# Kernel optimization log

Measured on AMD Instinct MI355X. Metric: run time of the kernel, lower is better.

Reference implementation:

```python
import jax, jax.numpy as jnp
import numpy as np

N_NODES = 100000
EPS = 1e-5


def gcn_conv(x, src, dst, W, b):
    # PyG GCNConv: h = W x; out_i = sum_{j->i} norm_ij * h_j  (with self-loops)
    h = x @ W  # [N, out]
    deg = jax.ops.segment_sum(jnp.ones_like(src, dtype=h.dtype), dst,
                              num_segments=N_NODES) + 1.0  # +1 self-loop
    dinv = jax.lax.rsqrt(deg)  # [N]
    norm = dinv[src] * dinv[dst]  # [E]
    msgs = h[src] * norm[:, None]  # [E, out]
    agg = jax.ops.segment_sum(msgs, dst, num_segments=N_NODES)
    agg = agg + h * (1.0 / deg)[:, None]  # self-loop term, norm = deg^-1
    return agg + b


def graph_norm(x, w, b, mean_scale):
    # PyG GraphNorm, single graph: normalize over nodes per feature
    mean = jnp.mean(x, axis=0, keepdims=True)
    xc = x - mean_scale * mean
    var = jnp.mean(xc * xc, axis=0, keepdims=True)
    return w * xc * jax.lax.rsqrt(var + EPS) + b


def layer_norm(x, w, b):
    mean = jnp.mean(x, axis=-1, keepdims=True)
    xc = x - mean
    var = jnp.mean(xc * xc, axis=-1, keepdims=True)
    return w * xc * jax.lax.rsqrt(var + EPS) + b


def setup_inputs() -> dict:
    key = jax.random.key(0)
    ks = jax.random.split(key, 8)
    in_dim, hid, emb = 128, 64, 32
    x = jax.random.normal(ks[0], (N_NODES, in_dim), dtype=jnp.float32)
    edge_index = jax.random.randint(ks[1], (2, 1600000), 0, N_NODES, dtype=jnp.int64)
    s = 0.05
    return {
        'x': x,
        'edge_index': edge_index,
        'W1': jax.random.normal(ks[2], (in_dim, hid), jnp.float32) * s,
        'b1': jnp.zeros((hid,), jnp.float32),
        'W2': jax.random.normal(ks[3], (hid, hid), jnp.float32) * s,
        'b2': jnp.zeros((hid,), jnp.float32),
        'gn_w': jnp.ones((hid,), jnp.float32),
        'gn_b': jnp.zeros((hid,), jnp.float32),
        'gn_ms': jnp.ones((hid,), jnp.float32),
        'ln_w': jnp.ones((hid,), jnp.float32),
        'ln_b': jnp.zeros((hid,), jnp.float32),
        'fc_W': jax.random.normal(ks[4], (hid, emb), jnp.float32) * s,
        'fc_b': jnp.zeros((emb,), jnp.float32),
    }


def reference(x, edge_index, W1, b1, W2, b2, gn_w, gn_b, gn_ms, ln_w, ln_b, fc_W, fc_b):
    src, dst = edge_index[0], edge_index[1]
    h = jax.nn.relu(gcn_conv(x, src, dst, W1, b1))
    h = graph_norm(h, gn_w, gn_b, gn_ms)
    h = layer_norm(h, ln_w, ln_b)
    # dropout: identity in eval mode
    h = jax.nn.relu(gcn_conv(h, src, dst, W2, b2))
    h = graph_norm(h, gn_w, gn_b, gn_ms)
    h = layer_norm(h, ln_w, ln_b)
    pooled = jnp.max(h, axis=0)  # [hid]
    embedding = pooled @ fc_W + fc_b  # [emb]; emb != 1 so no sigmoid
    return embedding
```

## Files before the change

kernel.cpp:

```cpp
#include <hip/hip_runtime.h>
#include <hip/hip_bf16.h>

#define EPSV 1e-5f
#define CHUNK 256
#define CAP 6144
#define MAXNB 512

typedef __attribute__((ext_vector_type(8))) short bf16x8;
typedef __attribute__((ext_vector_type(4))) float f32x4;

__device__ __forceinline__ ushort f2bf(float f) {
    union { float f; unsigned u; } c; c.f = f;
    unsigned u = c.u;
    return (ushort)((u + 0x7fffu + ((u >> 16) & 1u)) >> 16);
}
__device__ __forceinline__ float bf2f(ushort h) {
    union { unsigned u; float f; } c; c.u = ((unsigned)h) << 16;
    return c.f;
}
__device__ __forceinline__ float bflo(unsigned u) {
    union { unsigned u; float f; } c; c.u = u << 16;
    return c.f;
}
__device__ __forceinline__ float bfhi(unsigned u) {
    union { unsigned u; float f; } c; c.u = u & 0xFFFF0000u;
    return c.f;
}
__device__ __forceinline__ void acc8(float* a, uint4 u) {
    a[0] += bflo(u.x); a[1] += bfhi(u.x);
    a[2] += bflo(u.y); a[3] += bfhi(u.y);
    a[4] += bflo(u.z); a[5] += bfhi(u.z);
    a[6] += bflo(u.w); a[7] += bfhi(u.w);
}


__global__ void prep_kernel(const float* __restrict__ W1, const float* __restrict__ W2,
                            ushort* __restrict__ wsw1, ushort* __restrict__ wsw2,
                            int* __restrict__ bcur, int NB) {
    int t = blockIdx.x * blockDim.x + threadIdx.x;
    if (t < 128 * 64) {
        int k = t >> 6, n = t & 63;
        wsw1[((k >> 3) * 64 + n) * 8 + (k & 7)] = f2bf(W1[t]);
    }
    if (t < 64 * 64) {
        int k = t >> 6, n = t & 63;
        wsw2[((k >> 3) * 64 + n) * 8 + (k & 7)] = f2bf(W2[t]);
    }
    if (t < NB) bcur[t] = t * CAP;
}


#define EPB 8192

__global__ void __launch_bounds__(256) bucket_scatter(const int* __restrict__ ei,
                                                      int* __restrict__ bcur,
                                                      unsigned* __restrict__ bdata, int E,
                                                      int NB) {
    __shared__ int h[MAXNB];
    __shared__ int cur[MAXNB];
    int t = threadIdx.x;
    int base = blockIdx.x * EPB;
    int end = min(base + EPB, E);
    for (int b = t; b < NB; b += 256) h[b] = 0;
    __syncthreads();
    for (int e = base + t * 4; e < end; e += 1024) {
        int4 d4 = *reinterpret_cast<const int4*>(&ei[E + e]);
        atomicAdd(&h[d4.x >> 8], 1);
        atomicAdd(&h[d4.y >> 8], 1);
        atomicAdd(&h[d4.z >> 8], 1);
        atomicAdd(&h[d4.w >> 8], 1);
    }
    __syncthreads();
    for (int b = t; b < NB; b += 256) {
        int c = h[b];
        cur[b] = c ? atomicAdd(&bcur[b], c) : 0;
    }
    __syncthreads();
    for (int e = base + t * 4; e < end; e += 1024) {
        int4 s4 = *reinterpret_cast<const int4*>(&ei[e]);
        int4 d4 = *reinterpret_cast<const int4*>(&ei[E + e]);
        int p0 = atomicAdd(&cur[d4.x >> 8], 1);
        bdata[p0] = (unsigned)s4.x | ((unsigned)(d4.x & 255) << 20);
        int p1 = atomicAdd(&cur[d4.y >> 8], 1);
        bdata[p1] = (unsigned)s4.y | ((unsigned)(d4.y & 255) << 20);
        int p2 = atomicAdd(&cur[d4.z >> 8], 1);
        bdata[p2] = (unsigned)s4.z | ((unsigned)(d4.z & 255) << 20);
        int p3 = atomicAdd(&cur[d4.w >> 8], 1);
        bdata[p3] = (unsigned)s4.w | ((unsigned)(d4.w & 255) << 20);
    }
}


__global__ void __launch_bounds__(256) bucket_finish(const unsigned* __restrict__ bdata,
                                                     const int* __restrict__ bcur,
                                                     int2* __restrict__ NI,
                                                     float* __restrict__ dinv,
                                                     int* __restrict__ srcs, int N) {
    __shared__ int h[CHUNK];
    __shared__ int cur[CHUNK];
    int t = threadIdx.x;
    int beg = blockIdx.x * CAP;
    int end = bcur[blockIdx.x];
    h[t] = 0;
    __syncthreads();
    for (int e = beg + t; e < end; e += 256) atomicAdd(&h[bdata[e] >> 20], 1);
    __syncthreads();
    int deg = h[t];
    int pc = (deg + 3) & ~3;
    cur[t] = pc;
    __syncthreads();
    for (int off = 1; off < 256; off <<= 1) {
        int x = (t >= off) ? cur[t - off] : 0;
        __syncthreads();
        cur[t] += x;
        __syncthreads();
    }
    int begp = beg + cur[t] - pc;
    int node = blockIdx.x * CHUNK + t;
    if (node < N) {
        NI[node] = make_int2(begp, pc);
        dinv[node] = rsqrtf((float)deg + 1.0f);
    }
    h[t] = begp;
    __syncthreads();
    for (int e = beg + t; e < end; e += 256) {
        unsigned p = bdata[e];
        int pos = atomicAdd(&h[p >> 20], 1);
        srcs[pos] = (int)((p & 0xFFFFFu) << 3);
    }
    __syncthreads();
    int zr = N * 8;
    for (int k = h[t]; k < begp + pc; k++) srcs[k] = zr;
}


__global__ void __launch_bounds__(256) mm1_kernel(const float* __restrict__ X,
                                                  const ushort* __restrict__ wsw,
                                                  const float* __restrict__ dinv,
                                                  ushort* __restrict__ Ht, int N) {
    const int KO = 4;
    int w = threadIdx.x >> 6, lane = threadIdx.x & 63;
    int m = lane & 15, q = lane >> 4;
    int row = blockIdx.x * 64 + w * 16 + m;

    bf16x8 afrag[KO];
#pragma unroll
    for (int kk = 0; kk < KO; kk++) {
        float xv[8];
        if (row < N) {
            const float4* xp = reinterpret_cast<const float4*>(X + (size_t)row * 128 + kk * 32 + q * 8);
            float4 v0 = xp[0], v1 = xp[1];
            xv[0] = v0.x; xv[1] = v0.y; xv[2] = v0.z; xv[3] = v0.w;
            xv[4] = v1.x; xv[5] = v1.y; xv[6] = v1.z; xv[7] = v1.w;
        } else {
#pragma unroll
            for (int j = 0; j < 8; j++) xv[j] = 0.f;
        }
#pragma unroll
        for (int j = 0; j < 8; j++) afrag[kk][j] = (short)f2bf(xv[j]);
    }

    float dv[4];
#pragma unroll
    for (int reg = 0; reg < 4; reg++) {
        int r = blockIdx.x * 64 + w * 16 + q * 4 + reg;
        dv[reg] = (r < N) ? dinv[r] : 0.f;
    }

    const bf16x8* wp = reinterpret_cast<const bf16x8*>(wsw);
#pragma unroll
    for (int ct = 0; ct < 4; ct++) {
        f32x4 acc = {0.f, 0.f, 0.f, 0.f};
#pragma unroll
        for (int kk = 0; kk < KO; kk++) {
            bf16x8 b = wp[(kk * 4 + q) * 64 + ct * 16 + m];
            acc = __builtin_amdgcn_mfma_f32_16x16x32_bf16(afrag[kk], b, acc, 0, 0, 0);
        }
#pragma unroll
        for (int reg = 0; reg < 4; reg++) {
            int r = blockIdx.x * 64 + w * 16 + q * 4 + reg;
            if (r < N) Ht[(size_t)r * 64 + ct * 16 + m] = f2bf(acc[reg] * dv[reg]);
        }
    }
}


__global__ void __launch_bounds__(256) mm2_kernel(
    const ushort* __restrict__ A2, const ushort* __restrict__ wsw,
    const float* __restrict__ sums, const float* __restrict__ gn_w,
    const float* __restrict__ gn_b, const float* __restrict__ gn_ms,
    const float* __restrict__ ln_w, const float* __restrict__ ln_b,
    const float* __restrict__ dinv, ushort* __restrict__ Ht, int N) {
    __shared__ float sg[64], tg[64], lwv[64], lbv[64];
    int t = threadIdx.x;
    if (t < 64) {
        float invN = 1.0f / (float)N;
        float mean = sums[t] * invN;
        float m2 = sums[64 + t] * invN;
        float ms = gn_ms[t];
        float var = m2 - 2.f * ms * mean * mean + ms * ms * mean * mean;
        float s = gn_w[t] * rsqrtf(var + EPSV);
        sg[t] = s;
        tg[t] = gn_b[t] - s * ms * mean;
        lwv[t] = ln_w[t];
        lbv[t] = ln_b[t];
    }
    __syncthreads();

    int w = t >> 6, lane = t & 63;
    int m = lane & 15, q = lane >> 4;
    int row = blockIdx.x * 64 + w * 16 + m;

    float g[16];
#pragma unroll
    for (int kk = 0; kk < 2; kk++) {
        uint4 u = make_uint4(0, 0, 0, 0);
        if (row < N)
            u = *reinterpret_cast<const uint4*>(A2 + (size_t)row * 64 + kk * 32 + q * 8);
        unsigned uu[4] = {u.x, u.y, u.z, u.w};
#pragma unroll
        for (int p = 0; p < 4; p++) {
            int f0 = kk * 32 + q * 8 + 2 * p;
            g[kk * 8 + 2 * p] = sg[f0] * bflo(uu[p]) + tg[f0];
            g[kk * 8 + 2 * p + 1] = sg[f0 + 1] * bfhi(uu[p]) + tg[f0 + 1];
        }
    }
    float s1 = 0.f;
#pragma unroll
    for (int i = 0; i < 16; i++) s1 += g[i];
    s1 += __shfl_xor(s1, 16);
    s1 += __shfl_xor(s1, 32);
    float mu = s1 * (1.f / 64.f);
    float s2 = 0.f;
#pragma unroll
    for (int i = 0; i < 16; i++) {
        float c = g[i] - mu;
        s2 += c * c;
    }
    s2 += __shfl_xor(s2, 16);
    s2 += __shfl_xor(s2, 32);
    float rs = rsqrtf(s2 * (1.f / 64.f) + EPSV);

    bf16x8 afrag[2];
#pragma unroll
    for (int kk = 0; kk < 2; kk++) {
#pragma unroll
        for (int j = 0; j < 8; j++) {
            int f = kk * 32 + q * 8 + j;
            float y = lwv[f] * (g[kk * 8 + j] - mu) * rs + lbv[f];
            afrag[kk][j] = (short)f2bf(y);
        }
    }

    float dv[4];
#pragma unroll
    for (int reg = 0; reg < 4; reg++) {
        int r = blockIdx.x * 64 + w * 16 + q * 4 + reg;
        dv[reg] = (r < N) ? dinv[r] : 0.f;
    }

    const bf16x8* wp = reinterpret_cast<const bf16x8*>(wsw);
#pragma unroll
    for (int ct = 0; ct < 4; ct++) {
        f32x4 acc = {0.f, 0.f, 0.f, 0.f};
#pragma unroll
        for (int kk = 0; kk < 2; kk++) {
            bf16x8 b = wp[(kk * 4 + q) * 64 + ct * 16 + m];
            acc = __builtin_amdgcn_mfma_f32_16x16x32_bf16(afrag[kk], b, acc, 0, 0, 0);
        }
#pragma unroll
        for (int reg = 0; reg < 4; reg++) {
            int r = blockIdx.x * 64 + w * 16 + q * 4 + reg;
            if (r < N) Ht[(size_t)r * 64 + ct * 16 + m] = f2bf(acc[reg] * dv[reg]);
        }
    }
}


__global__ void __launch_bounds__(256) agg_kernel(
    const ushort* __restrict__ Ht, const int2* __restrict__ NI, const int* __restrict__ srcs,
    const float* __restrict__ dinv, const float* __restrict__ bias,
    ushort* __restrict__ out, float* __restrict__ sums, int N) {
    int t = threadIdx.x;
    int lane = t & 63;
    int g = lane >> 3, fq = lane & 7;
    int wid = (blockIdx.x * blockDim.x + t) >> 6;
    int nw = (gridDim.x * blockDim.x) >> 6;
    const uint4* H4 = reinterpret_cast<const uint4*>(Ht);
    uint4* O4 = reinterpret_cast<uint4*>(out);
    const int ZR = N * 8;
    float bb[8];
#pragma unroll
    for (int j = 0; j < 8; j++) bb[j] = bias[fq * 8 + j];
    float ps1[8] = {0, 0, 0, 0, 0, 0, 0, 0}, ps2[8] = {0, 0, 0, 0, 0, 0, 0, 0};

    for (int jo = wid; jo * 8 < N; jo += nw) {
        int node = jo * 8 + g;
        bool valid = node < N;
        int2 info = valid ? NI[node] : make_int2(0, 0);
        float di = valid ? dinv[node] : 0.f;
        int e = info.x, end = info.x + info.y;
        float a[8] = {0, 0, 0, 0, 0, 0, 0, 0};
        for (; e + 8 <= end; e += 8) {
            int4 i0 = *reinterpret_cast<const int4*>(&srcs[e]);
            int4 i1 = *reinterpret_cast<const int4*>(&srcs[e + 4]);
            uint4 u0 = H4[i0.x + fq];
            uint4 u1 = H4[i0.y + fq];
            uint4 u2 = H4[i0.z + fq];
            uint4 u3 = H4[i0.w + fq];
            uint4 u4 = H4[i1.x + fq];
            uint4 u5 = H4[i1.y + fq];
            uint4 u6 = H4[i1.z + fq];
            uint4 u7 = H4[i1.w + fq];
            acc8(a, u0); acc8(a, u1); acc8(a, u2); acc8(a, u3);
            acc8(a, u4); acc8(a, u5); acc8(a, u6); acc8(a, u7);
        }
        if (e < end) {
            int4 i0 = *reinterpret_cast<const int4*>(&srcs[e]);
            uint4 u0 = H4[i0.x + fq];
            uint4 u1 = H4[i0.y + fq];
            uint4 u2 = H4[i0.z + fq];
            uint4 u3 = H4[i0.w + fq];
            acc8(a, u0); acc8(a, u1); acc8(a, u2); acc8(a, u3);
        }
        uint4 us = H4[(valid ? node * 8 : ZR) + fq];
        float sf[8] = {bflo(us.x), bfhi(us.x), bflo(us.y), bfhi(us.y),
                       bflo(us.z), bfhi(us.z), bflo(us.w), bfhi(us.w)};
        float vv[8];
#pragma unroll
        for (int j = 0; j < 8; j++) vv[j] = fmaxf(di * a[j] + di * sf[j] + bb[j], 0.f);
        if (valid) {
            uint4 o;
            o.x = (unsigned)f2bf(vv[0]) | ((unsigned)f2bf(vv[1]) << 16);
            o.y = (unsigned)f2bf(vv[2]) | ((unsigned)f2bf(vv[3]) << 16);
            o.z = (unsigned)f2bf(vv[4]) | ((unsigned)f2bf(vv[5]) << 16);
            o.w = (unsigned)f2bf(vv[6]) | ((unsigned)f2bf(vv[7]) << 16);
            O4[(size_t)node * 8 + fq] = o;
#pragma unroll
            for (int j = 0; j < 8; j++) {
                ps1[j] += vv[j];
                ps2[j] += vv[j] * vv[j];
            }
        }
    }

    __shared__ float red[4][128];
    int wv = t >> 6;
#pragma unroll
    for (int j = 0; j < 8; j++) {
        float s = ps1[j], q = ps2[j];
        s += __shfl_xor(s, 8); s += __shfl_xor(s, 16); s += __shfl_xor(s, 32);
        q += __shfl_xor(q, 8); q += __shfl_xor(q, 16); q += __shfl_xor(q, 32);
        if (g == 0) {
            red[wv][fq * 8 + j] = s;
            red[wv][64 + fq * 8 + j] = q;
        }
    }
    __syncthreads();
    if (t < 128) {
        float v = red[0][t] + red[1][t] + red[2][t] + red[3][t];
        atomicAdd(&sums[t], v);
    }
}


__device__ __forceinline__ float gn_ln_row(float x, float mean, float var, float ms, float gw,
                                           float gb, float lw, float lb) {
    float g = gw * (x - ms * mean) * rsqrtf(var + EPSV) + gb;
    float mu = g;
#pragma unroll
    for (int off = 32; off; off >>= 1) mu += __shfl_xor(mu, off);
    mu *= (1.f / 64.f);
    float c = g - mu;
    float vv = c * c;
#pragma unroll
    for (int off = 32; off; off >>= 1) vv += __shfl_xor(vv, off);
    vv *= (1.f / 64.f);
    return lw * c * rsqrtf(vv + EPSV) + lb;
}

__device__ __forceinline__ unsigned fkey(float f) {
    unsigned u = __float_as_uint(f);
    return (u & 0x80000000u) ? ~u : (u | 0x80000000u);
}

__global__ void gnlnmax_kernel(const ushort* __restrict__ A, const float* __restrict__ sums,
                               const float* __restrict__ gn_w, const float* __restrict__ gn_b,
                               const float* __restrict__ gn_ms, const float* __restrict__ ln_w,
                               const float* __restrict__ ln_b, unsigned* __restrict__ pooled,
                               int N) {
    __shared__ float lmax[256];
    int lane = threadIdx.x & 63;
    int wave0 = (blockIdx.x * blockDim.x + threadIdx.x) >> 6;
    int nw = (gridDim.x * blockDim.x) >> 6;
    float invN = 1.0f / (float)N;
    float mean = sums[lane] * invN;
    float m2 = sums[64 + lane] * invN;
    float ms = gn_ms[lane];
    float var = m2 - 2.f * ms * mean * mean + ms * ms * mean * mean;
    float gw = gn_w[lane], gb = gn_b[lane], lw = ln_w[lane], lb = ln_b[lane];
    float mx = -3.4e38f;
    for (int i = wave0; i < N; i += nw) {
        float y = gn_ln_row(bf2f(A[(size_t)i * 64 + lane]), mean, var, ms, gw, gb, lw, lb);
        mx = fmaxf(mx, y);
    }
    lmax[threadIdx.x] = mx;
    __syncthreads();
    if (threadIdx.x < 64) {
        float m = fmaxf(fmaxf(lmax[threadIdx.x], lmax[threadIdx.x + 64]),
                        fmaxf(lmax[threadIdx.x + 128], lmax[threadIdx.x + 192]));
        atomicMax(&pooled[threadIdx.x], fkey(m));
    }
}


__global__ void final_kernel(const unsigned* __restrict__ pooled, const float* __restrict__ fc_W,
                             const float* __restrict__ fc_b, float* __restrict__ out) {
    __shared__ float p[64];
    int t = threadIdx.x;
    if (t < 64) {
        unsigned u = pooled[t];
        p[t] = (u & 0x80000000u) ? __uint_as_float(u ^ 0x80000000u) : __uint_as_float(~u);
    }
    __syncthreads();
    if (t < 32) {
        float acc = fc_b[t];
#pragma unroll
        for (int f = 0; f < 64; f++) acc += p[f] * fc_W[f * 32 + t];
        out[t] = acc;
    }
}


static inline size_t align_up(size_t v, size_t a) { return (v + a - 1) & ~(a - 1); }

extern "C" void kernel_launch(void* const* d_in, const int* in_sizes, int n_in, void* d_out,
                              int out_size, void* d_ws, size_t ws_size, hipStream_t stream) {
    const float* x = (const float*)d_in[0];
    const int* ei = (const int*)d_in[1];
    const float* W1 = (const float*)d_in[2];
    const float* b1 = (const float*)d_in[3];
    const float* W2 = (const float*)d_in[4];
    const float* b2 = (const float*)d_in[5];
    const float* gn_w = (const float*)d_in[6];
    const float* gn_b = (const float*)d_in[7];
    const float* gn_ms = (const float*)d_in[8];
    const float* ln_w = (const float*)d_in[9];
    const float* ln_b = (const float*)d_in[10];
    const float* fc_W = (const float*)d_in[11];
    const float* fc_b = (const float*)d_in[12];
    float* out = (float*)d_out;

    const int N = in_sizes[0] / 128;
    const int E = in_sizes[1] / 2;
    const int NB = (N + CHUNK - 1) / CHUNK;

    char* ws = (char*)d_ws;
    size_t off = 0;
    auto alloc = [&](size_t bytes) {
        char* p = ws + off;
        off = align_up(off + bytes, 256);
        return p;
    };
    int2* NI = (int2*)alloc((size_t)N * 8);
    int* bcur = (int*)alloc((size_t)(NB + 1) * 4);
    float* dinv = (float*)alloc((size_t)N * 4);
    unsigned* bdata = (unsigned*)alloc((size_t)NB * CAP * 4);
    int* srcs = (int*)alloc((size_t)NB * CAP * 4);
    ushort* bufB = (ushort*)alloc((size_t)N * 64 * 2);
    ushort* wsw1 = (ushort*)alloc(128 * 64 * 2);
    ushort* wsw2 = (ushort*)alloc(64 * 64 * 2);
    ushort* bufA = (ushort*)alloc((size_t)N * 64 * 2);
    size_t zoff = off;
    ushort* zrow = (ushort*)alloc(128);
    float* sums = (float*)alloc(256 * 4);
    unsigned* pooled = (unsigned*)alloc(64 * 4);
    size_t zlen = off - zoff;
    (void)zrow;

    hipMemsetAsync(ws + zoff, 0, zlen, stream);

    int nbB = (E + EPB - 1) / EPB;
    prep_kernel<<<48, 256, 0, stream>>>(W1, W2, wsw1, wsw2, bcur, NB);
    bucket_scatter<<<nbB, 256, 0, stream>>>(ei, bcur, bdata, E, NB);
    bucket_finish<<<NB, 256, 0, stream>>>(bdata, bcur, NI, dinv, srcs, N);

    int nbMM = (N + 63) / 64;
    int nbAgg = 782;

    mm1_kernel<<<nbMM, 256, 0, stream>>>(x, wsw1, dinv, bufA, N);
    agg_kernel<<<nbAgg, 256, 0, stream>>>(bufA, NI, srcs, dinv, b1, bufB, sums, N);

    mm2_kernel<<<nbMM, 256, 0, stream>>>(bufB, wsw2, sums, gn_w, gn_b, gn_ms, ln_w, ln_b, dinv,
                                         bufA, N);
    agg_kernel<<<nbAgg, 256, 0, stream>>>(bufA, NI, srcs, dinv, b2, bufB, sums + 128, N);
    gnlnmax_kernel<<<512, 256, 0, stream>>>(bufB, sums + 128, gn_w, gn_b, gn_ms, ln_w, ln_b,
                                            pooled, N);

    final_kernel<<<1, 64, 0, stream>>>(pooled, fc_W, fc_b, out);
}
```

Measured before the change: 305.3 us.

## Fuse final FC into pooling kernel, fold memset into prep, retune grids

The separate final kernel is removed. The last block of the pooling kernel, found with an atomic counter, now does the FC projection. The workspace memset is replaced by zeroing inside prep_kernel. The edge-scatter chunk size is reduced and the aggregation grid is now derived from N. The aim is fewer launches and better load balance, at the cost of more global atomics in the bucket scatter.

```diff
diff --git a/kernel.cpp b/kernel.cpp
--- a/kernel.cpp
+++ b/kernel.cpp
@@ -36,7 +36,8 @@
 
 __global__ void prep_kernel(const float* __restrict__ W1, const float* __restrict__ W2,
                             ushort* __restrict__ wsw1, ushort* __restrict__ wsw2,
-                            int* __restrict__ bcur, int NB) {
+                            int* __restrict__ bcur, int NB, int* __restrict__ zbase,
+                            int zwords) {
     int t = blockIdx.x * blockDim.x + threadIdx.x;
     if (t < 128 * 64) {
         int k = t >> 6, n = t & 63;
@@ -47,10 +48,11 @@
         wsw2[((k >> 3) * 64 + n) * 8 + (k & 7)] = f2bf(W2[t]);
     }
     if (t < NB) bcur[t] = t * CAP;
-}
-
-
-#define EPB 8192
+    if (t < zwords) zbase[t] = 0;
+}
+
+
+#define EPB 2048
 
 __global__ void __launch_bounds__(256) bucket_scatter(const int* __restrict__ ei,
                                                       int* __restrict__ bcur,
@@ -388,10 +390,14 @@
                                const float* __restrict__ gn_w, const float* __restrict__ gn_b,
                                const float* __restrict__ gn_ms, const float* __restrict__ ln_w,
                                const float* __restrict__ ln_b, unsigned* __restrict__ pooled,
-                               int N) {
+                               int* __restrict__ counter, const float* __restrict__ fc_W,
+                               const float* __restrict__ fc_b, float* __restrict__ out, int N) {
     __shared__ float lmax[256];
-    int lane = threadIdx.x & 63;
-    int wave0 = (blockIdx.x * blockDim.x + threadIdx.x) >> 6;
+    __shared__ float p[64];
+    __shared__ int isLast;
+    int t = threadIdx.x;
+    int lane = t & 63;
+    int wave0 = (blockIdx.x * blockDim.x + t) >> 6;
     int nw = (gridDim.x * blockDim.x) >> 6;
     float invN = 1.0f / (float)N;
     float mean = sums[lane] * invN;
@@ -404,30 +410,27 @@
         float y = gn_ln_row(bf2f(A[(size_t)i * 64 + lane]), mean, var, ms, gw, gb, lw, lb);
         mx = fmaxf(mx, y);
     }
-    lmax[threadIdx.x] = mx;
-    __syncthreads();
-    if (threadIdx.x < 64) {
-        float m = fmaxf(fmaxf(lmax[threadIdx.x], lmax[threadIdx.x + 64]),
-                        fmaxf(lmax[threadIdx.x + 128], lmax[threadIdx.x + 192]));
-        atomicMax(&pooled[threadIdx.x], fkey(m));
-    }
-}
-
-
-__global__ void final_kernel(const unsigned* __restrict__ pooled, const float* __restrict__ fc_W,
-                             const float* __restrict__ fc_b, float* __restrict__ out) {
-    __shared__ float p[64];
-    int t = threadIdx.x;
+    lmax[t] = mx;
+    __syncthreads();
     if (t < 64) {
-        unsigned u = pooled[t];
-        p[t] = (u & 0x80000000u) ? __uint_as_float(u ^ 0x80000000u) : __uint_as_float(~u);
-    }
-    __syncthreads();
-    if (t < 32) {
-        float acc = fc_b[t];
-#pragma unroll
-        for (int f = 0; f < 64; f++) acc += p[f] * fc_W[f * 32 + t];
-        out[t] = acc;
+        float m = fmaxf(fmaxf(lmax[t], lmax[t + 64]), fmaxf(lmax[t + 128], lmax[t + 192]));
+        atomicMax(&pooled[t], fkey(m));
+    }
+    __threadfence();
+    if (t == 0) isLast = (atomicAdd(counter, 1) == (int)gridDim.x - 1);
+    __syncthreads();
+    if (isLast) {
+        if (t < 64) {
+            unsigned u = atomicAdd(&pooled[t], 0u);
+            p[t] = (u & 0x80000000u) ? __uint_as_float(u ^ 0x80000000u) : __uint_as_float(~u);
+        }
+        __syncthreads();
+        if (t < 32) {
+            float acc = fc_b[t];
+#pragma unroll
+            for (int f = 0; f < 64; f++) acc += p[f] * fc_W[f * 32 + t];
+            out[t] = acc;
+        }
     }
 }
 
@@ -475,18 +478,20 @@
     ushort* zrow = (ushort*)alloc(128);
     float* sums = (float*)alloc(256 * 4);
     unsigned* pooled = (unsigned*)alloc(64 * 4);
+    int* counter = (int*)alloc(4);
     size_t zlen = off - zoff;
     (void)zrow;
-
-    hipMemsetAsync(ws + zoff, 0, zlen, stream);
+    int zwords = (int)(zlen / 4);
 
     int nbB = (E + EPB - 1) / EPB;
-    prep_kernel<<<48, 256, 0, stream>>>(W1, W2, wsw1, wsw2, bcur, NB);
+    prep_kernel<<<48, 256, 0, stream>>>(W1, W2, wsw1, wsw2, bcur, NB, (int*)(ws + zoff),
+                                        zwords);
     bucket_scatter<<<nbB, 256, 0, stream>>>(ei, bcur, bdata, E, NB);
     bucket_finish<<<NB, 256, 0, stream>>>(bdata, bcur, NI, dinv, srcs, N);
 
     int nbMM = (N + 63) / 64;
-    int nbAgg = 782;
+    int waves = (N + 7) / 8;
+    int nbAgg = (waves + 7) / 8;
 
     mm1_kernel<<<nbMM, 256, 0, stream>>>(x, wsw1, dinv, bufA, N);
     agg_kernel<<<nbAgg, 256, 0, stream>>>(bufA, NI, srcs, dinv, b1, bufB, sums, N);
@@ -495,7 +500,5 @@
                                          bufA, N);
     agg_kernel<<<nbAgg, 256, 0, stream>>>(bufA, NI, srcs, dinv, b2, bufB, sums + 128, N);
     gnlnmax_kernel<<<512, 256, 0, stream>>>(bufB, sums + 128, gn_w, gn_b, gn_ms, ln_w, ln_b,
-                                            pooled, N);
-
-    final_kernel<<<1, 64, 0, stream>>>(pooled, fc_W, fc_b, out);
-}
+                                            pooled, counter, fc_W, fc_b, out, N);
+}
```

Measured after the change: 365.1 us. 1.2x slower.

## Fold workspace zeroing into prep, transpose MFMA outputs, resize scatter and agg grids

Applied to the files above, without the earlier changes.

Replaces the hipMemsetAsync with zeroing inside prep_kernel, which removes one launch. The matmul kernels swap the MFMA operands so each lane owns one row, which lets it load a single dinv value and write packed 4-element bf16 stores instead of scattered 2-byte stores. Edges per scatter block drop from 8192 to 2048 to spread the work over more blocks. The agg grid now scales so each wave handles 8 nodes (about 3125 blocks instead of 782), which could change load balance or per-wave overhead.

```diff
diff --git a/kernel.cpp b/kernel.cpp
--- a/kernel.cpp
+++ b/kernel.cpp
@@ -36,7 +36,8 @@
 
 __global__ void prep_kernel(const float* __restrict__ W1, const float* __restrict__ W2,
                             ushort* __restrict__ wsw1, ushort* __restrict__ wsw2,
-                            int* __restrict__ bcur, int NB) {
+                            int* __restrict__ bcur, int NB, int* __restrict__ zbase,
+                            int zwords) {
     int t = blockIdx.x * blockDim.x + threadIdx.x;
     if (t < 128 * 64) {
         int k = t >> 6, n = t & 63;
@@ -47,10 +48,11 @@
         wsw2[((k >> 3) * 64 + n) * 8 + (k & 7)] = f2bf(W2[t]);
     }
     if (t < NB) bcur[t] = t * CAP;
-}
-
-
-#define EPB 8192
+    if (t < zwords) zbase[t] = 0;
+}
+
+
+#define EPB 2048
 
 __global__ void __launch_bounds__(256) bucket_scatter(const int* __restrict__ ei,
                                                       int* __restrict__ bcur,
@@ -140,15 +142,17 @@
                                                   ushort* __restrict__ Ht, int N) {
     const int KO = 4;
     int w = threadIdx.x >> 6, lane = threadIdx.x & 63;
-    int m = lane & 15, q = lane >> 4;
-    int row = blockIdx.x * 64 + w * 16 + m;
-
-    bf16x8 afrag[KO];
+    int n = lane & 15, q = lane >> 4;
+    int row = blockIdx.x * 64 + w * 16 + n;
+    bool valid = row < N;
+
+    bf16x8 bfrag[KO];
 #pragma unroll
     for (int kk = 0; kk < KO; kk++) {
         float xv[8];
-        if (row < N) {
-            const float4* xp = reinterpret_cast<const float4*>(X + (size_t)row * 128 + kk * 32 + q * 8);
+        if (valid) {
+            const float4* xp =
+                reinterpret_cast<const float4*>(X + (size_t)row * 128 + kk * 32 + q * 8);
             float4 v0 = xp[0], v1 = xp[1];
             xv[0] = v0.x; xv[1] = v0.y; xv[2] = v0.z; xv[3] = v0.w;
             xv[4] = v1.x; xv[5] = v1.y; xv[6] = v1.z; xv[7] = v1.w;
@@ -157,15 +161,10 @@
             for (int j = 0; j < 8; j++) xv[j] = 0.f;
         }
 #pragma unroll
-        for (int j = 0; j < 8; j++) afrag[kk][j] = (short)f2bf(xv[j]);
-    }
-
-    float dv[4];
-#pragma unroll
-    for (int reg = 0; reg < 4; reg++) {
-        int r = blockIdx.x * 64 + w * 16 + q * 4 + reg;
-        dv[reg] = (r < N) ? dinv[r] : 0.f;
-    }
+        for (int j = 0; j < 8; j++) bfrag[kk][j] = (short)f2bf(xv[j]);
+    }
+
+    float dv = valid ? dinv[row] : 0.f;
 
     const bf16x8* wp = reinterpret_cast<const bf16x8*>(wsw);
 #pragma unroll
@@ -173,13 +172,14 @@
         f32x4 acc = {0.f, 0.f, 0.f, 0.f};
 #pragma unroll
         for (int kk = 0; kk < KO; kk++) {
-            bf16x8 b = wp[(kk * 4 + q) * 64 + ct * 16 + m];
-            acc = __builtin_amdgcn_mfma_f32_16x16x32_bf16(afrag[kk], b, acc, 0, 0, 0);
-        }
-#pragma unroll
-        for (int reg = 0; reg < 4; reg++) {
-            int r = blockIdx.x * 64 + w * 16 + q * 4 + reg;
-            if (r < N) Ht[(size_t)r * 64 + ct * 16 + m] = f2bf(acc[reg] * dv[reg]);
+            bf16x8 a = wp[(kk * 4 + q) * 64 + ct * 16 + n];
+            acc = __builtin_amdgcn_mfma_f32_16x16x32_bf16(a, bfrag[kk], acc, 0, 0, 0);
+        }
+        if (valid) {
+            uint2 o;
+            o.x = (unsigned)f2bf(acc[0] * dv) | ((unsigned)f2bf(acc[1] * dv) << 16);
+            o.y = (unsigned)f2bf(acc[2] * dv) | ((unsigned)f2bf(acc[3] * dv) << 16);
+            *reinterpret_cast<uint2*>(&Ht[(size_t)row * 64 + ct * 16 + q * 4]) = o;
         }
     }
 }
@@ -208,14 +208,15 @@
     __syncthreads();
 
     int w = t >> 6, lane = t & 63;
-    int m = lane & 15, q = lane >> 4;
-    int row = blockIdx.x * 64 + w * 16 + m;
+    int n = lane & 15, q = lane >> 4;
+    int row = blockIdx.x * 64 + w * 16 + n;
+    bool valid = row < N;
 
     float g[16];
 #pragma unroll
     for (int kk = 0; kk < 2; kk++) {
         uint4 u = make_uint4(0, 0, 0, 0);
-        if (row < N)
+        if (valid)
             u = *reinterpret_cast<const uint4*>(A2 + (size_t)row * 64 + kk * 32 + q * 8);
         unsigned uu[4] = {u.x, u.y, u.z, u.w};
 #pragma unroll
@@ -241,23 +242,18 @@
     s2 += __shfl_xor(s2, 32);
     float rs = rsqrtf(s2 * (1.f / 64.f) + EPSV);
 
-    bf16x8 afrag[2];
+    bf16x8 bfrag[2];
 #pragma unroll
     for (int kk = 0; kk < 2; kk++) {
 #pragma unroll
         for (int j = 0; j < 8; j++) {
             int f = kk * 32 + q * 8 + j;
             float y = lwv[f] * (g[kk * 8 + j] - mu) * rs + lbv[f];
-            afrag[kk][j] = (short)f2bf(y);
-        }
-    }
-
-    float dv[4];
-#pragma unroll
-    for (int reg = 0; reg < 4; reg++) {
-        int r = blockIdx.x * 64 + w * 16 + q * 4 + reg;
-        dv[reg] = (r < N) ? dinv[r] : 0.f;
-    }
+            bfrag[kk][j] = (short)f2bf(y);
+        }
+    }
+
+    float dv = valid ? dinv[row] : 0.f;
 
     const bf16x8* wp = reinterpret_cast<const bf16x8*>(wsw);
 #pragma unroll
@@ -265,13 +261,14 @@
         f32x4 acc = {0.f, 0.f, 0.f, 0.f};
 #pragma unroll
         for (int kk = 0; kk < 2; kk++) {
-            bf16x8 b = wp[(kk * 4 + q) * 64 + ct * 16 + m];
-            acc = __builtin_amdgcn_mfma_f32_16x16x32_bf16(afrag[kk], b, acc, 0, 0, 0);
-        }
-#pragma unroll
-        for (int reg = 0; reg < 4; reg++) {
-            int r = blockIdx.x * 64 + w * 16 + q * 4 + reg;
-            if (r < N) Ht[(size_t)r * 64 + ct * 16 + m] = f2bf(acc[reg] * dv[reg]);
+            bf16x8 a = wp[(kk * 4 + q) * 64 + ct * 16 + n];
+            acc = __builtin_amdgcn_mfma_f32_16x16x32_bf16(a, bfrag[kk], acc, 0, 0, 0);
+        }
+        if (valid) {
+            uint2 o;
+            o.x = (unsigned)f2bf(acc[0] * dv) | ((unsigned)f2bf(acc[1] * dv) << 16);
+            o.y = (unsigned)f2bf(acc[2] * dv) | ((unsigned)f2bf(acc[3] * dv) << 16);
+            *reinterpret_cast<uint2*>(&Ht[(size_t)row * 64 + ct * 16 + q * 4]) = o;
         }
     }
 }
@@ -477,16 +474,17 @@
     unsigned* pooled = (unsigned*)alloc(64 * 4);
     size_t zlen = off - zoff;
     (void)zrow;
-
-    hipMemsetAsync(ws + zoff, 0, zlen, stream);
+    int zwords = (int)(zlen / 4);
 
     int nbB = (E + EPB - 1) / EPB;
-    prep_kernel<<<48, 256, 0, stream>>>(W1, W2, wsw1, wsw2, bcur, NB);
+    prep_kernel<<<48, 256, 0, stream>>>(W1, W2, wsw1, wsw2, bcur, NB, (int*)(ws + zoff),
+                                        zwords);
     bucket_scatter<<<nbB, 256, 0, stream>>>(ei, bcur, bdata, E, NB);
     bucket_finish<<<NB, 256, 0, stream>>>(bdata, bcur, NI, dinv, srcs, N);
 
     int nbMM = (N + 63) / 64;
-    int nbAgg = 782;
+    int waves = (N + 7) / 8;
+    int nbAgg = (waves + 3) / 4;
 
     mm1_kernel<<<nbMM, 256, 0, stream>>>(x, wsw1, dinv, bufA, N);
     agg_kernel<<<nbAgg, 256, 0, stream>>>(bufA, NI, srcs, dinv, b1, bufB, sums, N);
```

Measured after the change: 406.6 us. 33.2% more time.
